# Performance work log

Measured on AMD Instinct MI355X. Metric: run time of the kernel, lower is better.

## Reference

```python
import jax, jax.numpy as jnp
import numpy as np

B, S, V, E, H, L = 128, 2048, 800, 128, 64, 3  # batch, seq, vocab, embed, hidden, layers


def setup_inputs() -> dict:
    key = jax.random.key(0)
    ks = jax.random.split(key, 10)
    s = 0.08
    emb = jax.random.normal(ks[0], (V, E), jnp.float32) * s
    emb = emb.at[0].set(0.0)  # padding_idx=0 -> zero row
    # stacked RNN params: [layer, direction(0=fwd,1=bwd), ...]; all layer inputs are E==2*H==128
    w_ih = jax.random.normal(ks[1], (L, 2, H, E), jnp.float32) * s
    w_hh = jax.random.normal(ks[2], (L, 2, H, H), jnp.float32) * s
    b_ih = jax.random.normal(ks[3], (L, 2, H), jnp.float32) * s
    b_hh = jax.random.normal(ks[4], (L, 2, H), jnp.float32) * s
    fc1_w = jax.random.normal(ks[5], (128, 384), jnp.float32) * s
    fc1_b = jax.random.normal(ks[6], (128,), jnp.float32) * s
    fc2_w = jax.random.normal(ks[7], (1, 128), jnp.float32) * s
    fc2_b = jax.random.normal(ks[8], (1,), jnp.float32) * s
    x = jax.random.randint(ks[9], (B, S), 0, V, jnp.int32)
    return dict(x=x, emb=emb, w_ih=w_ih, w_hh=w_hh, b_ih=b_ih, b_hh=b_hh,
                fc1_w=fc1_w, fc1_b=fc1_b, fc2_w=fc2_w, fc2_b=fc2_b)


def _bidir_rnn(x, w_ih, w_hh, b_ih, b_hh):
    """3-layer bidirectional tanh RNN, PyTorch semantics (h0=0, eval: no dropout).
    Returns final hidden states (forward, backward) of the LAST layer."""
    h_f = h_b = None
    for l in range(L):
        outs = []
        finals = []
        for d, rev in ((0, False), (1, True)):
            # precompute input projection: [B,S,H]
            pre = jnp.einsum('bsd,hd->bsh', x, w_ih[l, d]) + b_ih[l, d] + b_hh[l, d]
            W = w_hh[l, d]

            def step(h, xt, W=W):
                h = jnp.tanh(xt + h @ W.T)
                return h, h

            h0 = jnp.zeros((x.shape[0], H), x.dtype)
            hT, ys = jax.lax.scan(step, h0, pre.transpose(1, 0, 2), reverse=rev)
            outs.append(ys.transpose(1, 0, 2))  # [B,S,H], time-ordered
            finals.append(hT)
        x = jnp.concatenate(outs, axis=-1)  # [B,S,2H] input to next layer
        h_f, h_b = finals
    return h_f, h_b


def reference(x, emb, w_ih, w_hh, b_ih, b_hh, fc1_w, fc1_b, fc2_w, fc2_b):
    xe = emb[x]  # [B,S,E]
    h_f, h_b = _bidir_rnn(xe, w_ih, w_hh, b_ih, b_hh)
    rnn_feat = jnp.concatenate([h_f, h_b], axis=1)        # [B,128] == h_n[-2],h_n[-1]
    mean_pool = xe.mean(axis=1)                           # [B,128]
    max_pool = xe.max(axis=1)                             # [B,128]
    combined = jnp.concatenate([rnn_feat, mean_pool, max_pool], axis=1)  # [B,384]
    # dropout layers are identity in eval mode
    h = jax.nn.relu(combined @ fc1_w.T + fc1_b)
    return h @ fc2_w.T + fc2_b  # [B,1]
```

## Files before the change

kernel.cpp:

```cpp
#include <hip/hip_runtime.h>
#include <math.h>

#define B 128
#define S 2048
#define V 800
#define E 128
#define H 64
#define NL 3
#define M (B*S)

typedef unsigned short ushort_t;

__device__ __forceinline__ float bf2f(unsigned short u){
  return __uint_as_float(((unsigned int)u) << 16);
}
__device__ __forceinline__ unsigned short f2bf(float f){
  unsigned int u = __float_as_uint(f);
  u += 0x7fff + ((u >> 16) & 1);
  return (unsigned short)(u >> 16);
}
__device__ __forceinline__ float fast_tanh(float x){
  float e = __expf(2.f*x);
  return 1.f - 2.f*__builtin_amdgcn_rcpf(e+1.f);
}
__device__ __forceinline__ int clamp_t(int t){
  return t < 0 ? 0 : (t > S-1 ? S-1 : t);
}

#define DPP_XOR1 0xB1
#define DPP_XOR2 0x4E
#define DPP_ROR4  0x124
#define DPP_ROR8  0x128
#define DPP_ROR12 0x12C
#define DPPI(v, ctrl) __builtin_amdgcn_update_dpp(0, (v), (ctrl), 0xf, 0xf, false)
#define DPPF(v, ctrl) __int_as_float(DPPI(__float_as_int(v), (ctrl)))
__device__ __forceinline__ float bperm(int addr, float v){
  return __int_as_float(__builtin_amdgcn_ds_bpermute(addr, __float_as_int(v)));
}
__device__ __host__ __forceinline__ constexpr int Gmask(int k){
  return (k & 3) | ((k & 4) << 2);
}

#if __has_builtin(__builtin_amdgcn_permlane32_swap)
#define HAVE_PL32 1
#else
#define HAVE_PL32 0
#endif
#if __has_builtin(__builtin_amdgcn_permlane16_swap)
#define HAVE_PL16 1
#else
#define HAVE_PL16 0
#endif

#if HAVE_PL32
#define XOR32F(x) ({ auto r_ = __builtin_amdgcn_permlane32_swap(__float_as_uint(x), __float_as_uint(x), false, false); \
                     __uint_as_float(pick32 ? r_[0] : r_[1]); })
#else
#define XOR32F(x) bperm(ba32, (x))
#endif
#if HAVE_PL16
#define XOR16F(x) ({ auto r_ = __builtin_amdgcn_permlane16_swap(__float_as_uint(x), __float_as_uint(x), false, false); \
                     __uint_as_float(pick16 ? r_[0] : r_[1]); })
#else
#define XOR16F(x) bperm(ba16, (x))
#endif

#define CALIB_AND_LOAD_W(wbase) do {                                         \
  int mk_ = i;                                                               \
  int g32m_;                                                                 \
  if (HAVE_PL32) {                                                           \
    auto r_ = __builtin_amdgcn_permlane32_swap((unsigned)mk_, (unsigned)mk_, false, false); \
    pick32 = ((int)r_[0] == (mk_ ^ 32));                                     \
    g32m_ = pick32 ? (int)r_[0] : (int)r_[1];                                \
  } else {                                                                   \
    g32m_ = mk_ ^ 32;                  \
  }                                                                          \
  if (HAVE_PL16) {                                                           \
    auto r_ = __builtin_amdgcn_permlane16_swap((unsigned)mk_, (unsigned)mk_, false, false); \
    pick16 = ((int)r_[0] == (mk_ ^ 16));                                     \
  }                                                                          \
  int cm_[8];                                                                \
  cm_[0]=mk_;   cm_[1]=DPPI(mk_,DPP_ROR4);                                   \
  cm_[2]=DPPI(mk_,DPP_ROR8);  cm_[3]=DPPI(mk_,DPP_ROR12);                    \
  cm_[4]=g32m_; cm_[5]=DPPI(g32m_,DPP_ROR4);                                 \
  cm_[6]=DPPI(g32m_,DPP_ROR8); cm_[7]=DPPI(g32m_,DPP_ROR12);                 \
  _Pragma("unroll")                                                          \
  for (int k=0;k<8;++k)                                                      \
    _Pragma("unroll")                                                        \
    for (int j=0;j<8;++j)                                                    \
      w[k*8+j] = (wbase)[(size_t)(i ^ Gmask(k))*H + cm_[j]];                 \
} while(0)

#define DOTJ(jj, hvj)                                                        \
  p0_=fmaf(w[0*8+jj],hvj,p0_); p1_=fmaf(w[1*8+jj],hvj,p1_);                  \
  p2_=fmaf(w[2*8+jj],hvj,p2_); p3_=fmaf(w[3*8+jj],hvj,p3_);                  \
  p4_=fmaf(w[4*8+jj],hvj,p4_); p5_=fmaf(w[5*8+jj],hvj,p5_);                  \
  p6_=fmaf(w[6*8+jj],hvj,p6_); p7_=fmaf(w[7*8+jj],hvj,p7_);

#define BSTEP(acc_expr)                                                      \
  {                                                                          \
    float hv0_ = h;                                                          \
    float hv1_ = DPPF(h, DPP_ROR4);                                          \
    float hv2_ = DPPF(h, DPP_ROR8);                                          \
    float hv3_ = DPPF(h, DPP_ROR12);                                         \
    float g_  = XOR32F(h);                                                   \
    float hv4_ = g_;                                                         \
    float hv5_ = DPPF(g_, DPP_ROR4);                                         \
    float hv6_ = DPPF(g_, DPP_ROR8);                                         \
    float hv7_ = DPPF(g_, DPP_ROR12);                                        \
    float p0_=(acc_expr), p1_=0.f,p2_=0.f,p3_=0.f,p4_=0.f,p5_=0.f,p6_=0.f,p7_=0.f; \
    DOTJ(0,hv0_); DOTJ(1,hv1_); DOTJ(2,hv2_); DOTJ(3,hv3_);                  \
    DOTJ(4,hv4_); DOTJ(5,hv5_); DOTJ(6,hv6_); DOTJ(7,hv7_);                  \
    p0_ += DPPF(p1_, DPP_XOR1); p2_ += DPPF(p3_, DPP_XOR1);                  \
    p4_ += DPPF(p5_, DPP_XOR1); p6_ += DPPF(p7_, DPP_XOR1);                  \
    p0_ += DPPF(p2_, DPP_XOR2); p4_ += DPPF(p6_, DPP_XOR2);                  \
    p0_ += XOR16F(p4_);                                                      \
    h = fast_tanh(p0_);                                                      \
  }

__global__ __launch_bounds__(128) void k_pre_emb(const float* __restrict__ emb,
    const float* __restrict__ w_ih, const float* __restrict__ b_ih, const float* __restrict__ b_hh,
    float* __restrict__ pe)
{
  const int v = blockIdx.x;
  const int n = threadIdx.x;
  const float* er = emb + (size_t)v*E;
  const float* wr = w_ih + (size_t)n*E;
  float acc = b_ih[n] + b_hh[n];
  #pragma unroll
  for (int e=0;e<E;e+=4){
    float4 ev = *(const float4*)(er+e);
    float4 wv = *(const float4*)(wr+e);
    acc = fmaf(ev.x, wv.x, acc);
    acc = fmaf(ev.y, wv.y, acc);
    acc = fmaf(ev.z, wv.z, acc);
    acc = fmaf(ev.w, wv.w, acc);
  }
  pe[(size_t)v*128 + n] = acc;
}

__global__ __launch_bounds__(128) void k_pool(const int* __restrict__ x, const float* __restrict__ emb,
      float* __restrict__ psum, float* __restrict__ pmax)
{
  const int b = blockIdx.x, c = blockIdx.y, e = threadIdx.x;
  const int* xb = x + (size_t)b*S + c*(S/16);
  float s=0.f, m=-INFINITY;
  for (int k=0;k<S/16;++k){
    int v = xb[k];
    float val = emb[(size_t)v*E + e];
    s += val; m = fmaxf(m,val);
  }
  psum[((size_t)b*16 + c)*E + e] = s;
  pmax[((size_t)b*16 + c)*E + e] = m;
}

__global__ __attribute__((amdgpu_flat_work_group_size(64,64)))
__attribute__((amdgpu_waves_per_eu(1,1)))
void k_rec0(const int* __restrict__ x,
            const float* __restrict__ pe,
            ushort_t* __restrict__ y,
            const float* __restrict__ w_hh,
            float* __restrict__ hfin)
{
  const int c = blockIdx.x;
  const int d = c >> 7;
  const int b = c & 127;
  const int i = threadIdx.x;
  float w[64];
  bool pick16=false, pick32=false;
  const int ba32 = (i^32)<<2, ba16 = (i^16)<<2;
  (void)ba32; (void)ba16;
  CALIB_AND_LOAD_W(w_hh + (size_t)d*H*H);
  const int* xb = x + (size_t)b*S;
  const float* peb = pe + d*H + i;
  ushort_t* yb = y + (size_t)b*S*(2*H) + d*H + i;
  const int fwd = (d==0);
  const int dt = fwd ? 1 : -1;
  int t = fwd ? 0 : S-1;

  int vx[8];
  #pragma unroll
  for (int k=0;k<8;++k) vx[k] = xb[clamp_t(t + k*dt)];
  float pl[4];
  #pragma unroll
  for (int k=0;k<4;++k) pl[k] = peb[(size_t)vx[k]*128];
  float h = 0.f;

#define STEP0(r) do {                                                        \
    float acc = pl[(r)&3];                                                   \
    pl[(r)&3] = peb[(size_t)vx[((r)+4)&7]*128];             \
    vx[(r)&7] = xb[clamp_t(t + 8*dt)];                       \
    BSTEP(acc);                                                              \
    yb[(size_t)t*(2*H)] = f2bf(h);                                           \
    t += dt;                                                                 \
  } while(0)

  for (int tq=0; tq<S; tq+=8){
    STEP0(0); STEP0(1); STEP0(2); STEP0(3);
    STEP0(4); STEP0(5); STEP0(6); STEP0(7);
  }
#undef STEP0
  hfin[((size_t)d*B + b)*H + i] = h;
}

template<int LAYER, int WRITEY>
__global__ __attribute__((amdgpu_flat_work_group_size(64,64)))
__attribute__((amdgpu_waves_per_eu(1,1)))
void k_rec(const float* __restrict__ pre,
           ushort_t* __restrict__ y,
           const float* __restrict__ w_hh,
           float* __restrict__ hfin)
{
  const int c = blockIdx.x;
  const int d = c >> 7;
  const int b = c & 127;
  const int i = threadIdx.x;
  float w[64];
  bool pick16=false, pick32=false;
  const int ba32 = (i^32)<<2, ba16 = (i^16)<<2;
  (void)ba32; (void)ba16;
  CALIB_AND_LOAD_W(w_hh + (size_t)(LAYER*2+d)*H*H);
  const float* pb = pre + ((size_t)d*M + (size_t)b*S)*H + i;
  ushort_t* yb = y + (size_t)b*S*(2*H) + d*H + i;
  const int fwd = (d==0);
  const int dt = fwd ? 1 : -1;
  int t = fwd ? 0 : S-1;

  float pl[8];
  #pragma unroll
  for (int k=0;k<8;++k) pl[k] = pb[(size_t)clamp_t(t + k*dt)*H];
  float h = 0.f;

#define STEPR(r) do {                                                        \
    float acc = pl[r];                                                       \
    pl[r] = pb[(size_t)clamp_t(t + 8*dt)*H];              \
    BSTEP(acc);                                                              \
    if (WRITEY) yb[(size_t)t*(2*H)] = f2bf(h);                               \
    t += dt;                                                                 \
  } while(0)

  for (int tq=0; tq<S; tq+=8){
    STEPR(0); STEPR(1); STEPR(2); STEPR(3);
    STEPR(4); STEPR(5); STEPR(6); STEPR(7);
  }
#undef STEPR
  hfin[((size_t)d*B + b)*H + i] = h;
}

#define KC 32
__global__ __launch_bounds__(256) void k_gemm(const ushort_t* __restrict__ Yin,
     const float* __restrict__ w_ih, const float* __restrict__ b_ih,
     const float* __restrict__ b_hh, float* __restrict__ pre, int layer)
{
  __shared__ float sY[KC][132];
  __shared__ float sW[KC][132];
  const int tid = threadIdx.x;
  const int m0 = blockIdx.x * 128;
  const int tn = (tid & 15) * 8;
  const int tm = (tid >> 4) * 8;
  float acc[8][8];
  #pragma unroll
  for (int a=0;a<8;++a)
    #pragma unroll
    for (int q=0;q<8;++q) acc[a][q]=0.f;
  const float* Wb = w_ih + (size_t)layer*2*H*E;
  for (int kc=0; kc<E; kc+=KC){
    #pragma unroll
    for (int r=0;r<2;++r){
      int idx = r*256 + tid;
      int ym = idx >> 2;
      int yk = (idx & 3)*8;
      const ushort_t* p = Yin + (size_t)(m0+ym)*E + kc + yk;
      ushort4 a = *(const ushort4*)p;
      ushort4 bq = *(const ushort4*)(p+4);
      sY[yk+0][ym]=bf2f(a.x);  sY[yk+1][ym]=bf2f(a.y);  sY[yk+2][ym]=bf2f(a.z);  sY[yk+3][ym]=bf2f(a.w);
      sY[yk+4][ym]=bf2f(bq.x); sY[yk+5][ym]=bf2f(bq.y); sY[yk+6][ym]=bf2f(bq.z); sY[yk+7][ym]=bf2f(bq.w);
    }
    #pragma unroll
    for (int r=0;r<4;++r){
      int idx = r*256 + tid;
      int wn = idx >> 3;
      int wk = (idx & 7)*4;
      float4 v = *(const float4*)(Wb + (size_t)wn*E + kc + wk);
      sW[wk+0][wn]=v.x; sW[wk+1][wn]=v.y; sW[wk+2][wn]=v.z; sW[wk+3][wn]=v.w;
    }
    __syncthreads();
    #pragma unroll 4
    for (int k=0;k<KC;++k){
      float4 a0 = *(const float4*)&sY[k][tm];
      float4 a1 = *(const float4*)&sY[k][tm+4];
      float4 b0 = *(const float4*)&sW[k][tn];
      float4 b1 = *(const float4*)&sW[k][tn+4];
      float am[8]={a0.x,a0.y,a0.z,a0.w,a1.x,a1.y,a1.z,a1.w};
      float bn[8]={b0.x,b0.y,b0.z,b0.w,b1.x,b1.y,b1.z,b1.w};
      #pragma unroll
      for (int mi=0;mi<8;++mi)
        #pragma unroll
        for (int ni=0;ni<8;++ni)
          acc[mi][ni] = fmaf(am[mi], bn[ni], acc[mi][ni]);
    }
    __syncthreads();
  }
  const int d = tn >> 6;
  const int i0 = tn & 63;
  float bias[8];
  #pragma unroll
  for (int ni=0;ni<8;++ni)
    bias[ni] = b_ih[(size_t)(layer*2+d)*H + i0+ni] + b_hh[(size_t)(layer*2+d)*H + i0+ni];
  #pragma unroll
  for (int mi=0;mi<8;++mi){
    size_t off = ((size_t)d*M + (m0+tm+mi))*H + i0;
    float4 o0 = make_float4(acc[mi][0]+bias[0], acc[mi][1]+bias[1], acc[mi][2]+bias[2], acc[mi][3]+bias[3]);
    float4 o1 = make_float4(acc[mi][4]+bias[4], acc[mi][5]+bias[5], acc[mi][6]+bias[6], acc[mi][7]+bias[7]);
    *(float4*)(pre + off)     = o0;
    *(float4*)(pre + off + 4) = o1;
  }
}

__global__ __launch_bounds__(128) void k_fc(const float* __restrict__ psum, const float* __restrict__ pmax,
    const float* __restrict__ hfin, const float* __restrict__ fc1_w, const float* __restrict__ fc1_b,
    const float* __restrict__ fc2_w, const float* __restrict__ fc2_b, float* __restrict__ out)
{
  const int b = blockIdx.x, tid = threadIdx.x;
  __shared__ __align__(16) float comb[384];
  __shared__ float red[2];
  float s=0.f, m=-INFINITY;
  #pragma unroll
  for (int c=0;c<16;++c){
    s += psum[((size_t)b*16+c)*E + tid];
    m = fmaxf(m, pmax[((size_t)b*16+c)*E + tid]);
  }
  comb[128+tid] = s*(1.f/2048.f);
  comb[256+tid] = m;
  comb[tid] = (tid<64) ? hfin[(size_t)b*H + tid] : hfin[((size_t)B + b)*H + (tid-64)];
  __syncthreads();
  float acc = fc1_b[tid];
  const float4* wrow = (const float4*)(fc1_w + (size_t)tid*384);
  const float4* cb = (const float4*)comb;
  #pragma unroll 8
  for (int k=0;k<96;++k){
    float4 wv = wrow[k]; float4 cv = cb[k];
    acc = fmaf(wv.x,cv.x,acc); acc = fmaf(wv.y,cv.y,acc);
    acc = fmaf(wv.z,cv.z,acc); acc = fmaf(wv.w,cv.w,acc);
  }
  acc = fmaxf(acc, 0.f);
  float p = acc * fc2_w[tid];
  #pragma unroll
  for (int off=32; off>0; off>>=1) p += __shfl_down(p, off);
  if ((tid & 63)==0) red[tid>>6] = p;
  __syncthreads();
  if (tid==0) out[b] = red[0] + red[1] + fc2_b[0];
}

extern "C" void kernel_launch(void* const* d_in, const int* in_sizes, int n_in,
                              void* d_out, int out_size, void* d_ws, size_t ws_size,
                              hipStream_t stream)
{
  const int*   x     = (const int*)  d_in[0];
  const float* emb   = (const float*)d_in[1];
  const float* w_ih  = (const float*)d_in[2];
  const float* w_hh  = (const float*)d_in[3];
  const float* b_ih  = (const float*)d_in[4];
  const float* b_hh  = (const float*)d_in[5];
  const float* fc1_w = (const float*)d_in[6];
  const float* fc1_b = (const float*)d_in[7];
  const float* fc2_w = (const float*)d_in[8];
  const float* fc2_b = (const float*)d_in[9];
  float* out = (float*)d_out;

  char* ws = (char*)d_ws;
  float*    pre  = (float*)(ws);
  ushort_t* y    = (ushort_t*)(ws + (size_t)2*M*H*4);
  float*    pe   = (float*)(ws + (size_t)2*M*H*4 + (size_t)M*128*2);
  float*    psum = pe   + (size_t)V*128;
  float*    pmax = psum + (size_t)B*16*E;
  float*    hfin = pmax + (size_t)B*16*E;

  k_pre_emb<<<V, 128, 0, stream>>>(emb, w_ih, b_ih, b_hh, pe);
  k_pool<<<dim3(B,16), 128, 0, stream>>>(x, emb, psum, pmax);
  k_rec0<<<256, 64, 0, stream>>>(x, pe, y, w_hh, hfin);
  k_gemm<<<M/128, 256, 0, stream>>>(y, w_ih, b_ih, b_hh, pre, 1);
  k_rec<1,1><<<256, 64, 0, stream>>>(pre, y, w_hh, hfin);
  k_gemm<<<M/128, 256, 0, stream>>>(y, w_ih, b_ih, b_hh, pre, 2);
  k_rec<2,0><<<256, 64, 0, stream>>>(pre, y, w_hh, hfin);
  k_fc<<<B, 128, 0, stream>>>(psum, pmax, hfin, fc1_w, fc1_b, fc2_w, fc2_b, out);
}
```

Measured before the change: 1.580 ms.

## Interleave forward and backward recurrences in one wave per batch row

```diff
diff --git a/kernel.cpp b/kernel.cpp
--- a/kernel.cpp
+++ b/kernel.cpp
@@ -65,7 +65,7 @@
 #define XOR16F(x) bperm(ba16, (x))
 #endif
 
-#define CALIB_AND_LOAD_W(wbase) do {                                         \
+#define CALIB() do {                                                         \
   int mk_ = i;                                                               \
   int g32m_;                                                                 \
   if (HAVE_PL32) {                                                           \
@@ -73,49 +73,51 @@
     pick32 = ((int)r_[0] == (mk_ ^ 32));                                     \
     g32m_ = pick32 ? (int)r_[0] : (int)r_[1];                                \
   } else {                                                                   \
-    g32m_ = mk_ ^ 32;                  \
+    g32m_ = mk_ ^ 32;                                                        \
   }                                                                          \
   if (HAVE_PL16) {                                                           \
     auto r_ = __builtin_amdgcn_permlane16_swap((unsigned)mk_, (unsigned)mk_, false, false); \
     pick16 = ((int)r_[0] == (mk_ ^ 16));                                     \
   }                                                                          \
-  int cm_[8];                                                                \
-  cm_[0]=mk_;   cm_[1]=DPPI(mk_,DPP_ROR4);                                   \
-  cm_[2]=DPPI(mk_,DPP_ROR8);  cm_[3]=DPPI(mk_,DPP_ROR12);                    \
-  cm_[4]=g32m_; cm_[5]=DPPI(g32m_,DPP_ROR4);                                 \
-  cm_[6]=DPPI(g32m_,DPP_ROR8); cm_[7]=DPPI(g32m_,DPP_ROR12);                 \
+  cm[0]=mk_;   cm[1]=DPPI(mk_,DPP_ROR4);                                     \
+  cm[2]=DPPI(mk_,DPP_ROR8);  cm[3]=DPPI(mk_,DPP_ROR12);                      \
+  cm[4]=g32m_; cm[5]=DPPI(g32m_,DPP_ROR4);                                   \
+  cm[6]=DPPI(g32m_,DPP_ROR8); cm[7]=DPPI(g32m_,DPP_ROR12);                   \
+} while(0)
+
+#define LOAD_W8(wreg, wbase) do {                                            \
   _Pragma("unroll")                                                          \
   for (int k=0;k<8;++k)                                                      \
     _Pragma("unroll")                                                        \
     for (int j=0;j<8;++j)                                                    \
-      w[k*8+j] = (wbase)[(size_t)(i ^ Gmask(k))*H + cm_[j]];                 \
+      wreg[k*8+j] = (wbase)[(size_t)(i ^ Gmask(k))*H + cm[j]];               \
 } while(0)
 
-#define DOTJ(jj, hvj)                                                        \
-  p0_=fmaf(w[0*8+jj],hvj,p0_); p1_=fmaf(w[1*8+jj],hvj,p1_);                  \
-  p2_=fmaf(w[2*8+jj],hvj,p2_); p3_=fmaf(w[3*8+jj],hvj,p3_);                  \
-  p4_=fmaf(w[4*8+jj],hvj,p4_); p5_=fmaf(w[5*8+jj],hvj,p5_);                  \
-  p6_=fmaf(w[6*8+jj],hvj,p6_); p7_=fmaf(w[7*8+jj],hvj,p7_);
-
-#define BSTEP(acc_expr)                                                      \
+#define DOTJX(wX, jj, hvj)                                                   \
+  p0_=fmaf(wX[0*8+jj],hvj,p0_); p1_=fmaf(wX[1*8+jj],hvj,p1_);                \
+  p2_=fmaf(wX[2*8+jj],hvj,p2_); p3_=fmaf(wX[3*8+jj],hvj,p3_);                \
+  p4_=fmaf(wX[4*8+jj],hvj,p4_); p5_=fmaf(wX[5*8+jj],hvj,p5_);                \
+  p6_=fmaf(wX[6*8+jj],hvj,p6_); p7_=fmaf(wX[7*8+jj],hvj,p7_);
+
+#define BSTEPX(hX, wX, acc_expr)                                             \
   {                                                                          \
-    float hv0_ = h;                                                          \
-    float hv1_ = DPPF(h, DPP_ROR4);                                          \
-    float hv2_ = DPPF(h, DPP_ROR8);                                          \
-    float hv3_ = DPPF(h, DPP_ROR12);                                         \
-    float g_  = XOR32F(h);                                                   \
+    float hv0_ = hX;                                                         \
+    float hv1_ = DPPF(hX, DPP_ROR4);                                         \
+    float hv2_ = DPPF(hX, DPP_ROR8);                                         \
+    float hv3_ = DPPF(hX, DPP_ROR12);                                        \
+    float g_  = XOR32F(hX);                                                  \
     float hv4_ = g_;                                                         \
     float hv5_ = DPPF(g_, DPP_ROR4);                                         \
     float hv6_ = DPPF(g_, DPP_ROR8);                                         \
     float hv7_ = DPPF(g_, DPP_ROR12);                                        \
     float p0_=(acc_expr), p1_=0.f,p2_=0.f,p3_=0.f,p4_=0.f,p5_=0.f,p6_=0.f,p7_=0.f; \
-    DOTJ(0,hv0_); DOTJ(1,hv1_); DOTJ(2,hv2_); DOTJ(3,hv3_);                  \
-    DOTJ(4,hv4_); DOTJ(5,hv5_); DOTJ(6,hv6_); DOTJ(7,hv7_);                  \
+    DOTJX(wX,0,hv0_); DOTJX(wX,1,hv1_); DOTJX(wX,2,hv2_); DOTJX(wX,3,hv3_);  \
+    DOTJX(wX,4,hv4_); DOTJX(wX,5,hv5_); DOTJX(wX,6,hv6_); DOTJX(wX,7,hv7_);  \
     p0_ += DPPF(p1_, DPP_XOR1); p2_ += DPPF(p3_, DPP_XOR1);                  \
     p4_ += DPPF(p5_, DPP_XOR1); p6_ += DPPF(p7_, DPP_XOR1);                  \
     p0_ += DPPF(p2_, DPP_XOR2); p4_ += DPPF(p6_, DPP_XOR2);                  \
     p0_ += XOR16F(p4_);                                                      \
-    h = fast_tanh(p0_);                                                      \
+    hX = fast_tanh(p0_);                                                     \
   }
 
 __global__ __launch_bounds__(128) void k_pre_emb(const float* __restrict__ emb,
@@ -162,45 +164,65 @@
             const float* __restrict__ w_hh,
             float* __restrict__ hfin)
 {
-  const int c = blockIdx.x;
-  const int d = c >> 7;
-  const int b = c & 127;
+  const int b = blockIdx.x;
   const int i = threadIdx.x;
-  float w[64];
   bool pick16=false, pick32=false;
+  int cm[8];
   const int ba32 = (i^32)<<2, ba16 = (i^16)<<2;
   (void)ba32; (void)ba16;
-  CALIB_AND_LOAD_W(w_hh + (size_t)d*H*H);
+  CALIB();
+  float wA[64], wB[64];
+  LOAD_W8(wA, w_hh + (size_t)0*H*H);
+  LOAD_W8(wB, w_hh + (size_t)1*H*H);
   const int* xb = x + (size_t)b*S;
-  const float* peb = pe + d*H + i;
-  ushort_t* yb = y + (size_t)b*S*(2*H) + d*H + i;
-  const int fwd = (d==0);
-  const int dt = fwd ? 1 : -1;
-  int t = fwd ? 0 : S-1;
-
-  int vx[8];
-  #pragma unroll
-  for (int k=0;k<8;++k) vx[k] = xb[clamp_t(t + k*dt)];
-  float pl[4];
-  #pragma unroll
-  for (int k=0;k<4;++k) pl[k] = peb[(size_t)vx[k]*128];
-  float h = 0.f;
-
-#define STEP0(r) do {                                                        \
-    float acc = pl[(r)&3];                                                   \
-    pl[(r)&3] = peb[(size_t)vx[((r)+4)&7]*128];             \
-    vx[(r)&7] = xb[clamp_t(t + 8*dt)];                       \
-    BSTEP(acc);                                                              \
-    yb[(size_t)t*(2*H)] = f2bf(h);                                           \
-    t += dt;                                                                 \
+  const float* peA = pe + i;
+  const float* peB = pe + 64 + i;
+  ushort_t* yA = y + (size_t)b*S*128 + i;
+  ushort_t* yB = y + (size_t)b*S*128 + 64 + i;
+  int tA = 0, tB = S-1;
+
+  int vxA[8], vxB[8];
+  #pragma unroll
+  for (int k=0;k<8;++k){ vxA[k] = xb[k]; vxB[k] = xb[S-1-k]; }
+  float plA[4], plB[4];
+  #pragma unroll
+  for (int k=0;k<4;++k){
+    plA[k] = peA[(size_t)vxA[k]*128];
+    plB[k] = peB[(size_t)vxB[k]*128];
+  }
+  float hA = 0.f, hB = 0.f;
+
+#define STEP0A(r) do {                                                       \
+    float acc = plA[(r)&3];                                                  \
+    plA[(r)&3] = peA[(size_t)vxA[((r)+4)&7]*128];                            \
+    vxA[(r)&7] = xb[clamp_t(tA + 8)];                                        \
+    BSTEPX(hA, wA, acc);                                                     \
+    yA[(size_t)tA*128] = f2bf(hA);                                           \
+    tA += 1;                                                                 \
   } while(0)
+#define STEP0B(r) do {                                                       \
+    float acc = plB[(r)&3];                                                  \
+    plB[(r)&3] = peB[(size_t)vxB[((r)+4)&7]*128];                            \
+    vxB[(r)&7] = xb[clamp_t(tB - 8)];                                        \
+    BSTEPX(hB, wB, acc);                                                     \
+    yB[(size_t)tB*128] = f2bf(hB);                                           \
+    tB -= 1;                                                                 \
+  } while(0)
 
   for (int tq=0; tq<S; tq+=8){
-    STEP0(0); STEP0(1); STEP0(2); STEP0(3);
-    STEP0(4); STEP0(5); STEP0(6); STEP0(7);
-  }
-#undef STEP0
-  hfin[((size_t)d*B + b)*H + i] = h;
+    STEP0A(0); STEP0B(0);
+    STEP0A(1); STEP0B(1);
+    STEP0A(2); STEP0B(2);
+    STEP0A(3); STEP0B(3);
+    STEP0A(4); STEP0B(4);
+    STEP0A(5); STEP0B(5);
+    STEP0A(6); STEP0B(6);
+    STEP0A(7); STEP0B(7);
+  }
+#undef STEP0A
+#undef STEP0B
+  hfin[(size_t)b*H + i]       = hA;
+  hfin[((size_t)B + b)*H + i] = hB;
 }
 
 template<int LAYER, int WRITEY>
@@ -211,40 +233,59 @@
            const float* __restrict__ w_hh,
            float* __restrict__ hfin)
 {
-  const int c = blockIdx.x;
-  const int d = c >> 7;
-  const int b = c & 127;
+  const int b = blockIdx.x;
   const int i = threadIdx.x;
-  float w[64];
   bool pick16=false, pick32=false;
+  int cm[8];
   const int ba32 = (i^32)<<2, ba16 = (i^16)<<2;
   (void)ba32; (void)ba16;
-  CALIB_AND_LOAD_W(w_hh + (size_t)(LAYER*2+d)*H*H);
-  const float* pb = pre + ((size_t)d*M + (size_t)b*S)*H + i;
-  ushort_t* yb = y + (size_t)b*S*(2*H) + d*H + i;
-  const int fwd = (d==0);
-  const int dt = fwd ? 1 : -1;
-  int t = fwd ? 0 : S-1;
-
-  float pl[8];
-  #pragma unroll
-  for (int k=0;k<8;++k) pl[k] = pb[(size_t)clamp_t(t + k*dt)*H];
-  float h = 0.f;
-
-#define STEPR(r) do {                                                        \
-    float acc = pl[r];                                                       \
-    pl[r] = pb[(size_t)clamp_t(t + 8*dt)*H];              \
-    BSTEP(acc);                                                              \
-    if (WRITEY) yb[(size_t)t*(2*H)] = f2bf(h);                               \
-    t += dt;                                                                 \
+  CALIB();
+  float wA[64], wB[64];
+  LOAD_W8(wA, w_hh + (size_t)(LAYER*2+0)*H*H);
+  LOAD_W8(wB, w_hh + (size_t)(LAYER*2+1)*H*H);
+  const float* pA = pre + ((size_t)b*S)*H + i;
+  const float* pB = pre + ((size_t)M + (size_t)b*S)*H + i;
+  ushort_t* yA = y + (size_t)b*S*128 + i;
+  ushort_t* yB = y + (size_t)b*S*128 + 64 + i;
+  int tA = 0, tB = S-1;
+
+  float plA[8], plB[8];
+  #pragma unroll
+  for (int k=0;k<8;++k){
+    plA[k] = pA[(size_t)k*H];
+    plB[k] = pB[(size_t)(S-1-k)*H];
+  }
+  float hA = 0.f, hB = 0.f;
+
+#define STEPRA(r) do {                                                       \
+    float acc = plA[r];                                                      \
+    plA[r] = pA[(size_t)clamp_t(tA + 8)*H];                                  \
+    BSTEPX(hA, wA, acc);                                                     \
+    if (WRITEY) yA[(size_t)tA*128] = f2bf(hA);                               \
+    tA += 1;                                                                 \
   } while(0)
+#define STEPRB(r) do {                                                       \
+    float acc = plB[r];                                                      \
+    plB[r] = pB[(size_t)clamp_t(tB - 8)*H];                                  \
+    BSTEPX(hB, wB, acc);                                                     \
+    if (WRITEY) yB[(size_t)tB*128] = f2bf(hB);                               \
+    tB -= 1;                                                                 \
+  } while(0)
 
   for (int tq=0; tq<S; tq+=8){
-    STEPR(0); STEPR(1); STEPR(2); STEPR(3);
-    STEPR(4); STEPR(5); STEPR(6); STEPR(7);
-  }
-#undef STEPR
-  hfin[((size_t)d*B + b)*H + i] = h;
+    STEPRA(0); STEPRB(0);
+    STEPRA(1); STEPRB(1);
+    STEPRA(2); STEPRB(2);
+    STEPRA(3); STEPRB(3);
+    STEPRA(4); STEPRB(4);
+    STEPRA(5); STEPRB(5);
+    STEPRA(6); STEPRB(6);
+    STEPRA(7); STEPRB(7);
+  }
+#undef STEPRA
+#undef STEPRB
+  hfin[(size_t)b*H + i]       = hA;
+  hfin[((size_t)B + b)*H + i] = hB;
 }
 
 #define KC 32
@@ -378,10 +419,10 @@
 
   k_pre_emb<<<V, 128, 0, stream>>>(emb, w_ih, b_ih, b_hh, pe);
   k_pool<<<dim3(B,16), 128, 0, stream>>>(x, emb, psum, pmax);
-  k_rec0<<<256, 64, 0, stream>>>(x, pe, y, w_hh, hfin);
+  k_rec0<<<B, 64, 0, stream>>>(x, pe, y, w_hh, hfin);
   k_gemm<<<M/128, 256, 0, stream>>>(y, w_ih, b_ih, b_hh, pre, 1);
-  k_rec<1,1><<<256, 64, 0, stream>>>(pre, y, w_hh, hfin);
+  k_rec<1,1><<<B, 64, 0, stream>>>(pre, y, w_hh, hfin);
   k_gemm<<<M/128, 256, 0, stream>>>(y, w_ih, b_ih, b_hh, pre, 2);
-  k_rec<2,0><<<256, 64, 0, stream>>>(pre, y, w_hh, hfin);
+  k_rec<2,0><<<B, 64, 0, stream>>>(pre, y, w_hh, hfin);
   k_fc<<<B, 128, 0, stream>>>(psum, pmax, hfin, fc1_w, fc1_b, fc2_w, fc2_b, out);
 }
```

New measurement: 2.805 ms. 1.77x slower.
